# Kernel tuning notes

Hardware: AMD Instinct MI355X
Metric: run time of the kernel (lower is better)

The kernel has to match this reference:

```python
import jax, jax.numpy as jnp
import numpy as np

N_NODES = 50000
N_EDGES = 600000
D_IN = 128
D_OUT = 128
LN_EPS = 1e-5
LEAKY_SLOPE = 0.2


def setup_inputs() -> dict:
    key = jax.random.key(0)
    k1, k2, k3, k4 = jax.random.split(key, 4)
    x = jax.random.normal(k1, (N_NODES, D_IN), dtype=jnp.float32)
    edge_index = jax.random.randint(k2, (2, N_EDGES), 0, N_NODES, dtype=jnp.int64)
    # xavier_uniform with gain for relu (sqrt(2))
    gain = float(np.sqrt(2.0))
    lim_w = gain * np.sqrt(6.0 / (D_IN + D_OUT))
    W_lin = jax.random.uniform(k3, (D_OUT, D_IN), minval=-lim_w, maxval=lim_w, dtype=jnp.float32)
    lim_a = gain * np.sqrt(6.0 / (2 * D_OUT + 1))
    a = jax.random.uniform(k4, (2 * D_OUT,), minval=-lim_a, maxval=lim_a, dtype=jnp.float32)
    gamma = jnp.ones((D_OUT,), dtype=jnp.float32)
    beta = jnp.zeros((D_OUT,), dtype=jnp.float32)
    return {"x": x, "edge_index": edge_index, "W_lin": W_lin, "a": a,
            "gamma": gamma, "beta": beta}


def reference(x, edge_index, W_lin, a, gamma, beta):
    N = x.shape[0]
    h = x @ W_lin.T                                  # [N, D_OUT]
    d = h.shape[1]
    # attention MLP on concat([h_src, h_dst]) == h_src@a[:d] + h_dst@a[d:]
    s_src = h @ a[:d]                                # [N]
    s_dst = h @ a[d:]                                # [N]
    src, dst = edge_index[0], edge_index[1]
    e = jax.nn.leaky_relu(s_src[src] + s_dst[dst], LEAKY_SLOPE)   # [E]
    # segment softmax over destination nodes (numerically stable)
    m = jax.ops.segment_max(e, dst, num_segments=N)               # [N], -inf for empty
    ex = jnp.exp(e - m[dst])                                      # [E]
    z = jax.ops.segment_sum(ex, dst, num_segments=N)              # [N]
    alpha = ex / z[dst]                                           # [E]
    # weighted scatter-add of source messages
    msgs = h[src] * alpha[:, None]                                # [E, D_OUT]
    agg = jax.ops.segment_sum(msgs, dst, num_segments=N)          # [N, D_OUT]
    # residual (input_dim == output_dim -> identity projection) + LayerNorm
    y = agg + x
    mu = jnp.mean(y, axis=-1, keepdims=True)
    var = jnp.mean(jnp.square(y - mu), axis=-1, keepdims=True)
    return (y - mu) * jax.lax.rsqrt(var + LN_EPS) * gamma + beta
```

## Files before the change

### kernel.cpp

```cpp
#include <hip/hip_runtime.h>
#include <hip/hip_bf16.h>

typedef unsigned short u16;
typedef unsigned int   u32;
typedef __bf16 bf16x8 __attribute__((ext_vector_type(8)));
typedef float  f32x4  __attribute__((ext_vector_type(4)));

#define D 128
#define CPAD 16

__device__ inline float bflo(u32 u) { return __builtin_bit_cast(float, u << 16); }
__device__ inline float bfhi(u32 u) { return __builtin_bit_cast(float, u & 0xffff0000u); }
__device__ inline float bfu(u16 u)  { return __builtin_bit_cast(float, ((u32)u) << 16); }
__device__ inline u16 f2bf(float f) {
    __hip_bfloat16 b = __float2bfloat16(f);
    return __builtin_bit_cast(u16, b);
}

__device__ inline int detect_f32(const u32* __restrict__ x32, int lane) {
    u32 v = x32[lane];
    u32 elo = (v >> 7) & 0xFFu;
    return __popcll(__ballot(elo >= 150u)) >= 4;
}
__device__ inline int detect_i64(const int* __restrict__ ei32, int lane) {
    return __popcll(__ballot(ei32[2 * lane + 1] != 0)) < 8;
}

#define LWP 136

__global__ __launch_bounds__(256) void k_gemm(const void* __restrict__ xv,
                                              const void* __restrict__ Wv,
                                              const void* __restrict__ av,
                                              const int* __restrict__ ei,
                                              u16* __restrict__ h,
                                              float* __restrict__ s_src,
                                              float* __restrict__ s_dst,
                                              int* __restrict__ cnt,
                                              u32* __restrict__ scode,
                                              int N, int E)
{
    __shared__ u16 lw[128 * LWP];
    const int tid  = threadIdx.x;
    const int wave = tid >> 6;
    const int lane = tid & 63;
    const int quad = lane >> 4;
    const int l16  = lane & 15;
    const int m0   = blockIdx.x * 64 + wave * 16;

    const int f32 = detect_f32((const u32*)xv, lane);
    const int i64 = detect_i64(ei, lane);

    const int gtid = blockIdx.x * 256 + tid;
    const int TT   = gridDim.x * 256;
    int dk[3], tk[3];
#pragma unroll
    for (int k = 0; k < 3; ++k) {
        int e = gtid + k * TT;
        dk[k] = 0;
        if (e < E) {
            if (i64) dk[k] = ((const int2*)ei)[E + e].x;
            else     dk[k] = ei[E + e];
        }
    }
#pragma unroll
    for (int k = 0; k < 3; ++k) {
        int e = gtid + k * TT;
        tk[k] = 64;
        if (e < E) tk[k] = atomicAdd(cnt + (size_t)dk[k] * CPAD, 1);
    }

    if (f32) {
        const float* Wf = (const float*)Wv;
#pragma unroll
        for (int it = 0; it < 8; ++it) {
            int i = it * 256 + tid;
            int row = i >> 4, blk = i & 15;
            const float* src = Wf + row * D + blk * 8;
            f32x4 v0 = *(const f32x4*)src;
            f32x4 v1 = *(const f32x4*)(src + 4);
            union { u16 u[8]; uint4 q; } t;
#pragma unroll
            for (int j = 0; j < 4; ++j) { t.u[j] = f2bf(v0[j]); t.u[4 + j] = f2bf(v1[j]); }
            *(uint4*)&lw[row * LWP + blk * 8] = t.q;
        }
    } else {
        const u16* Wu = (const u16*)Wv;
#pragma unroll
        for (int it = 0; it < 8; ++it) {
            int i = it * 256 + tid;
            int row = i >> 4, blk = i & 15;
            *(uint4*)&lw[row * LWP + blk * 8] = *(const uint4*)(Wu + row * D + blk * 8);
        }
    }

    int arow = m0 + l16;
    if (arow > N - 1) arow = N - 1;

    bf16x8 afrag[4];
    if (f32) {
        const float* xr = (const float*)xv + (size_t)arow * D + quad * 8;
#pragma unroll
        for (int s = 0; s < 4; ++s) {
            f32x4 v0 = *(const f32x4*)(xr + s * 32);
            f32x4 v1 = *(const f32x4*)(xr + s * 32 + 4);
            union { u16 u[8]; bf16x8 v; } t;
#pragma unroll
            for (int j = 0; j < 4; ++j) { t.u[j] = f2bf(v0[j]); t.u[4 + j] = f2bf(v1[j]); }
            afrag[s] = t.v;
        }
    } else {
        const u16* xr = (const u16*)xv + (size_t)arow * D + quad * 8;
#pragma unroll
        for (int s = 0; s < 4; ++s)
            afrag[s] = __builtin_bit_cast(bf16x8, *(const uint4*)(xr + s * 32));
    }

    __syncthreads();

    f32x4 acc[8] = {};
#pragma unroll
    for (int t = 0; t < 8; ++t) {
#pragma unroll
        for (int s = 0; s < 4; ++s) {
            bf16x8 b = __builtin_bit_cast(bf16x8,
                *(const uint4*)&lw[(t * 16 + l16) * LWP + quad * 8 + s * 32]);
            acc[t] = __builtin_amdgcn_mfma_f32_16x16x32_bf16(afrag[s], b, acc[t], 0, 0, 0);
        }
    }

    float as[8], ad[8];
    if (f32) {
        const float* af = (const float*)av;
#pragma unroll
        for (int t = 0; t < 8; ++t) { as[t] = af[t * 16 + l16]; ad[t] = af[D + t * 16 + l16]; }
    } else {
        const u16* au = (const u16*)av;
#pragma unroll
        for (int t = 0; t < 8; ++t) { as[t] = bfu(au[t * 16 + l16]); ad[t] = bfu(au[D + t * 16 + l16]); }
    }

#pragma unroll
    for (int i = 0; i < 4; ++i) {
        int r = m0 + quad * 4 + i;
        float ps = 0.f, pd = 0.f;
#pragma unroll
        for (int t = 0; t < 8; ++t) {
            float v = acc[t][i];
            ps += v * as[t];
            pd += v * ad[t];
        }
#pragma unroll
        for (int m = 1; m < 16; m <<= 1) {
            ps += __shfl_xor(ps, m, 64);
            pd += __shfl_xor(pd, m, 64);
        }
        if (r < N) {
            if (l16 == 0) { s_src[r] = ps; s_dst[r] = pd; }
            u16* hrow = h + (size_t)r * D + l16;
#pragma unroll
            for (int t = 0; t < 8; ++t)
                hrow[t * 16] = f2bf(acc[t][i]);
        }
    }

#pragma unroll
    for (int k = 0; k < 3; ++k) {
        int e = gtid + k * TT;
        if (e < E)
            scode[e] = (tk[k] < 64) ? (u32)(dk[k] * 64 + tk[k]) : 0xFFFFFFFFu;
    }
}

__global__ __launch_bounds__(256) void k_edge(const int* __restrict__ ei,
                                              const float* __restrict__ s_src,
                                              const float* __restrict__ s_dst,
                                              const u32* __restrict__ scode,
                                              u32* __restrict__ bkt, int E)
{
    const int lane = threadIdx.x & 63;
    const int i64 = detect_i64(ei, lane);
    int e = blockIdx.x * 256 + threadIdx.x;
    if (e >= E) return;

    u32 code = scode[e];
    int src, dst;
    if (i64) {
        src = ((const int2*)ei)[e].x;
        dst = ((const int2*)ei)[E + e].x;
    } else {
        src = ei[e]; dst = ei[E + e];
    }
    float sv = s_src[src] + s_dst[dst];
    float lr = sv > 0.f ? sv : 0.2f * sv;
    float ex = __expf(lr);
    if (code != 0xFFFFFFFFu)
        bkt[code] = (u32)(src & 0xFFFF) | ((u32)f2bf(ex) << 16);
}

__global__ __launch_bounds__(256) void k_agg(const u16* __restrict__ h,
                                             const void* __restrict__ xv,
                                             const int* __restrict__ cnt,
                                             const u32* __restrict__ bkt,
                                             const void* __restrict__ gv_,
                                             const void* __restrict__ bv_,
                                             void* __restrict__ outv, int N)
{
    const int lane = threadIdx.x & 63;
    const int f32 = detect_f32((const u32*)xv, lane);
    const int wave = threadIdx.x >> 6;
    const int quad = lane >> 4;
    const int l16  = lane & 15;
    const int n = blockIdx.x * 4 + wave;
    if (n >= N) return;

    float xr_[8], g[8], bb[8];
    if (f32) {
        const float* xr = (const float*)xv + (size_t)n * D + l16 * 8;
        const float* gr = (const float*)gv_ + l16 * 8;
        const float* br = (const float*)bv_ + l16 * 8;
#pragma unroll
        for (int k = 0; k < 8; ++k) { xr_[k] = xr[k]; g[k] = gr[k]; bb[k] = br[k]; }
    } else {
        uint4 xq = *(const uint4*)((const u16*)xv + (size_t)n * D + l16 * 8);
        uint4 gq = *(const uint4*)((const u16*)gv_ + l16 * 8);
        uint4 bq = *(const uint4*)((const u16*)bv_ + l16 * 8);
        const u32 xw[4] = {xq.x, xq.y, xq.z, xq.w};
        const u32 gw[4] = {gq.x, gq.y, gq.z, gq.w};
        const u32 bw[4] = {bq.x, bq.y, bq.z, bq.w};
#pragma unroll
        for (int k = 0; k < 4; ++k) {
            xr_[2*k] = bflo(xw[k]); xr_[2*k+1] = bfhi(xw[k]);
            g[2*k]   = bflo(gw[k]); g[2*k+1]   = bfhi(gw[k]);
            bb[2*k]  = bflo(bw[k]); bb[2*k+1]  = bfhi(bw[k]);
        }
    }

    int d = cnt[(size_t)n * CPAD]; if (d > 64) d = 64;
    d = __builtin_amdgcn_readfirstlane(d);
    const int ng = (d + 3) >> 2;
    const u32* slots = bkt + n * 64;

    u32 pk[8];
#pragma unroll
    for (int k = 0; k < 8; ++k)
        if (k < ng) pk[k] = slots[4 * k + quad];

    uint4 hv[8];
    float w[8];
#pragma unroll
    for (int k = 0; k < 8; ++k) {
        if (k < ng) {
            bool act = (4 * k + quad) < d;
            u32 p = act ? pk[k] : 0u;
            w[k] = act ? bfhi(pk[k]) : 0.f;
            hv[k] = *(const uint4*)(h + (size_t)(p & 0xFFFFu) * D + l16 * 8);
        }
    }

    float acc[8] = {};
    float zs = 0.f;
#pragma unroll
    for (int k = 0; k < 8; ++k) {
        if (k < ng) {
            float wk = w[k];
            uint4 q = hv[k];
            zs += wk;
            acc[0] += wk * bflo(q.x); acc[1] += wk * bfhi(q.x);
            acc[2] += wk * bflo(q.y); acc[3] += wk * bfhi(q.y);
            acc[4] += wk * bflo(q.z); acc[5] += wk * bfhi(q.z);
            acc[6] += wk * bflo(q.w); acc[7] += wk * bfhi(q.w);
        }
    }

    int j = 32;
    for (; j + 4 <= d; j += 4) {
        u32 pkk = slots[j + quad];
        float wk = bfhi(pkk);
        uint4 q = *(const uint4*)(h + (size_t)(pkk & 0xFFFFu) * D + l16 * 8);
        zs += wk;
        acc[0] += wk * bflo(q.x); acc[1] += wk * bfhi(q.x);
        acc[2] += wk * bflo(q.y); acc[3] += wk * bfhi(q.y);
        acc[4] += wk * bflo(q.z); acc[5] += wk * bfhi(q.z);
        acc[6] += wk * bflo(q.w); acc[7] += wk * bfhi(q.w);
    }
    if (j + quad < d) {
        u32 pkk = slots[j + quad];
        float wk = bfhi(pkk);
        uint4 q = *(const uint4*)(h + (size_t)(pkk & 0xFFFFu) * D + l16 * 8);
        zs += wk;
        acc[0] += wk * bflo(q.x); acc[1] += wk * bfhi(q.x);
        acc[2] += wk * bflo(q.y); acc[3] += wk * bfhi(q.y);
        acc[4] += wk * bflo(q.z); acc[5] += wk * bfhi(q.z);
        acc[6] += wk * bflo(q.w); acc[7] += wk * bfhi(q.w);
    }

#pragma unroll
    for (int k = 0; k < 8; ++k) {
        acc[k] += __shfl_xor(acc[k], 16, 64);
        acc[k] += __shfl_xor(acc[k], 32, 64);
    }
    zs += __shfl_xor(zs, 16, 64);
    zs += __shfl_xor(zs, 32, 64);
    float inv = d > 0 ? 1.f / zs : 0.f;

    float y[8];
#pragma unroll
    for (int k = 0; k < 8; ++k) y[k] = acc[k] * inv + xr_[k];

    float s1 = 0.f, s2 = 0.f;
#pragma unroll
    for (int k = 0; k < 8; ++k) { s1 += y[k]; s2 += y[k] * y[k]; }
#pragma unroll
    for (int m = 1; m < 16; m <<= 1) {
        s1 += __shfl_xor(s1, m, 64);
        s2 += __shfl_xor(s2, m, 64);
    }
    float mu  = s1 * (1.f / 128.f);
    float var = s2 * (1.f / 128.f) - mu * mu;
    float r   = rsqrtf(var + 1e-5f);

    if (quad == 0) {
        if (f32) {
            float* orow = (float*)outv + (size_t)n * D + l16 * 8;
            f32x4 o0, o1;
#pragma unroll
            for (int k = 0; k < 4; ++k) o0[k] = (y[k] - mu) * r * g[k] + bb[k];
#pragma unroll
            for (int k = 0; k < 4; ++k) o1[k] = (y[4+k] - mu) * r * g[4+k] + bb[4+k];
            *(f32x4*)orow = o0;
            *(f32x4*)(orow + 4) = o1;
        } else {
            uint4 pkq;
            u32 wq[4];
#pragma unroll
            for (int k = 0; k < 4; ++k) {
                float o0 = (y[2*k]   - mu) * r * g[2*k]   + bb[2*k];
                float o1 = (y[2*k+1] - mu) * r * g[2*k+1] + bb[2*k+1];
                wq[k] = (u32)f2bf(o0) | ((u32)f2bf(o1) << 16);
            }
            pkq.x = wq[0]; pkq.y = wq[1]; pkq.z = wq[2]; pkq.w = wq[3];
            *(uint4*)((u16*)outv + (size_t)n * D + l16 * 8) = pkq;
        }
    }
}

extern "C" void kernel_launch(void* const* d_in, const int* in_sizes, int n_in,
                              void* d_out, int out_size, void* d_ws, size_t ws_size,
                              hipStream_t stream)
{
    const void* x  = d_in[0];
    const int*  ei = (const int*)d_in[1];
    const void* W  = d_in[2];
    const void* a  = d_in[3];
    const void* gm = d_in[4];
    const void* bt = d_in[5];

    const int N = in_sizes[0] / D;
    const int E = in_sizes[1] / 2;

    char* ws = (char*)d_ws;
    size_t off = 0;
    u16*   h     = (u16*)(ws + off);   off += (size_t)N * D * sizeof(u16);
    float* ssrc  = (float*)(ws + off); off += (size_t)N * sizeof(float);
    float* sdst  = (float*)(ws + off); off += (size_t)N * sizeof(float);
    int*   cnt   = (int*)(ws + off);   off += (size_t)N * CPAD * sizeof(int);
    u32*   bkt   = (u32*)(ws + off);   off += (size_t)N * 64 * sizeof(u32);
    u32*   scode = (u32*)(ws + off);   off += (size_t)E * sizeof(u32);

    hipMemsetAsync(cnt, 0, (size_t)N * CPAD * sizeof(int), stream);
    k_gemm <<<(N + 63) / 64,   256, 0, stream>>>(x, W, a, ei, h, ssrc, sdst, cnt, scode, N, E);
    k_edge <<<(E + 255) / 256, 256, 0, stream>>>(ei, ssrc, sdst, scode, bkt, E);
    k_agg  <<<(N + 3) / 4,     256, 0, stream>>>(h, x, cnt, bkt, gm, bt, d_out, N);
}
```

Measured before the change: 166.6 us.

## Fuse memset, GEMM, edge and aggregation into one cooperative persistent kernel

```diff
diff --git a/kernel.cpp b/kernel.cpp
--- a/kernel.cpp
+++ b/kernel.cpp
@@ -1,5 +1,8 @@
 #include <hip/hip_runtime.h>
 #include <hip/hip_bf16.h>
+#include <hip/hip_cooperative_groups.h>
+
+namespace cg = cooperative_groups;
 
 typedef unsigned short u16;
 typedef unsigned int   u32;
@@ -8,6 +11,8 @@
 
 #define D 128
 #define CPAD 16
+#define LWP 136
+#define EK 8
 
 __device__ inline float bflo(u32 u) { return __builtin_bit_cast(float, u << 16); }
 __device__ inline float bfhi(u32 u) { return __builtin_bit_cast(float, u & 0xffff0000u); }
@@ -26,7 +31,313 @@
     return __popcll(__ballot(ei32[2 * lane + 1] != 0)) < 8;
 }
 
-#define LWP 136
+__global__ __launch_bounds__(256) void k_fused(
+    const void* __restrict__ xv, const void* __restrict__ Wv,
+    const void* __restrict__ av, const int* __restrict__ ei,
+    const void* __restrict__ gv_, const void* __restrict__ bv_,
+    void* __restrict__ outv,
+    u16* __restrict__ h, float* __restrict__ s_src, float* __restrict__ s_dst,
+    int* __restrict__ cnt, u32* __restrict__ bkt, int N, int E)
+{
+    __shared__ u16 lw[128 * LWP];
+    const int tid  = threadIdx.x;
+    const int wave = tid >> 6;
+    const int lane = tid & 63;
+    const int quad = lane >> 4;
+    const int l16  = lane & 15;
+    const int G    = gridDim.x;
+    const int gtid = blockIdx.x * 256 + tid;
+    const int TT   = G * 256;
+
+    const int f32 = detect_f32((const u32*)xv, lane);
+    const int i64 = detect_i64(ei, lane);
+
+    for (int ci = gtid; ci < (N * CPAD) >> 2; ci += TT) {
+        int4 z = {0, 0, 0, 0};
+        *(int4*)(cnt + (size_t)ci * 4) = z;
+    }
+    __threadfence();
+    cg::this_grid().sync();
+    __threadfence();
+
+    int dd[EK];
+#pragma unroll
+    for (int k = 0; k < EK; ++k) {
+        int e = gtid + k * TT;
+        dd[k] = 0;
+        if (e < E) dd[k] = i64 ? ((const int2*)ei)[E + e].x : ei[E + e];
+    }
+    int tk[EK];
+#pragma unroll
+    for (int k = 0; k < EK; ++k) {
+        int e = gtid + k * TT;
+        tk[k] = 64;
+        if (e < E) tk[k] = atomicAdd(cnt + (size_t)dd[k] * CPAD, 1);
+    }
+
+    const int TILES = (N + 63) >> 6;
+    bool staged = false;
+    for (int tile = blockIdx.x; tile < TILES; tile += G) {
+        if (!staged) {
+            staged = true;
+            if (f32) {
+                const float* Wf = (const float*)Wv;
+#pragma unroll
+                for (int it = 0; it < 8; ++it) {
+                    int i = it * 256 + tid;
+                    int row = i >> 4, blk = i & 15;
+                    const float* src = Wf + row * D + blk * 8;
+                    f32x4 v0 = *(const f32x4*)src;
+                    f32x4 v1 = *(const f32x4*)(src + 4);
+                    union { u16 u[8]; uint4 q; } t;
+#pragma unroll
+                    for (int j = 0; j < 4; ++j) { t.u[j] = f2bf(v0[j]); t.u[4 + j] = f2bf(v1[j]); }
+                    *(uint4*)&lw[row * LWP + blk * 8] = t.q;
+                }
+            } else {
+                const u16* Wu = (const u16*)Wv;
+#pragma unroll
+                for (int it = 0; it < 8; ++it) {
+                    int i = it * 256 + tid;
+                    int row = i >> 4, blk = i & 15;
+                    *(uint4*)&lw[row * LWP + blk * 8] = *(const uint4*)(Wu + row * D + blk * 8);
+                }
+            }
+        }
+
+        int m0 = tile * 64 + wave * 16;
+        int arow = m0 + l16;
+        if (arow > N - 1) arow = N - 1;
+
+        bf16x8 afrag[4];
+        if (f32) {
+            const float* xr = (const float*)xv + (size_t)arow * D + quad * 8;
+#pragma unroll
+            for (int s = 0; s < 4; ++s) {
+                f32x4 v0 = *(const f32x4*)(xr + s * 32);
+                f32x4 v1 = *(const f32x4*)(xr + s * 32 + 4);
+                union { u16 u[8]; bf16x8 v; } t;
+#pragma unroll
+                for (int j = 0; j < 4; ++j) { t.u[j] = f2bf(v0[j]); t.u[4 + j] = f2bf(v1[j]); }
+                afrag[s] = t.v;
+            }
+        } else {
+            const u16* xr = (const u16*)xv + (size_t)arow * D + quad * 8;
+#pragma unroll
+            for (int s = 0; s < 4; ++s)
+                afrag[s] = __builtin_bit_cast(bf16x8, *(const uint4*)(xr + s * 32));
+        }
+
+        __syncthreads();
+
+        f32x4 acc[8] = {};
+#pragma unroll
+        for (int t = 0; t < 8; ++t) {
+#pragma unroll
+            for (int s = 0; s < 4; ++s) {
+                bf16x8 b = __builtin_bit_cast(bf16x8,
+                    *(const uint4*)&lw[(t * 16 + l16) * LWP + quad * 8 + s * 32]);
+                acc[t] = __builtin_amdgcn_mfma_f32_16x16x32_bf16(afrag[s], b, acc[t], 0, 0, 0);
+            }
+        }
+
+        float as[8], ad[8];
+        if (f32) {
+            const float* af = (const float*)av;
+#pragma unroll
+            for (int t = 0; t < 8; ++t) { as[t] = af[t * 16 + l16]; ad[t] = af[D + t * 16 + l16]; }
+        } else {
+            const u16* au = (const u16*)av;
+#pragma unroll
+            for (int t = 0; t < 8; ++t) { as[t] = bfu(au[t * 16 + l16]); ad[t] = bfu(au[D + t * 16 + l16]); }
+        }
+
+#pragma unroll
+        for (int i = 0; i < 4; ++i) {
+            int r = m0 + quad * 4 + i;
+            float ps = 0.f, pd = 0.f;
+#pragma unroll
+            for (int t = 0; t < 8; ++t) {
+                float v = acc[t][i];
+                ps += v * as[t];
+                pd += v * ad[t];
+            }
+#pragma unroll
+            for (int m = 1; m < 16; m <<= 1) {
+                ps += __shfl_xor(ps, m, 64);
+                pd += __shfl_xor(pd, m, 64);
+            }
+            if (r < N) {
+                if (l16 == 0) { s_src[r] = ps; s_dst[r] = pd; }
+                u16* hrow = h + (size_t)r * D + l16;
+#pragma unroll
+                for (int t = 0; t < 8; ++t)
+                    hrow[t * 16] = f2bf(acc[t][i]);
+            }
+        }
+    }
+    __threadfence();
+    cg::this_grid().sync();
+    __threadfence();
+
+#pragma unroll
+    for (int k = 0; k < EK; ++k) {
+        int e = gtid + k * TT;
+        if (e < E) {
+            int src, dst;
+            if (i64) {
+                src = ((const int2*)ei)[e].x;
+                dst = ((const int2*)ei)[E + e].x;
+            } else {
+                src = ei[e]; dst = ei[E + e];
+            }
+            float sv = s_src[src] + s_dst[dst];
+            float lr = sv > 0.f ? sv : 0.2f * sv;
+            float ex = __expf(lr);
+            if (tk[k] < 64)
+                bkt[(size_t)dst * 64 + tk[k]] = (u32)(src & 0xFFFF) | ((u32)f2bf(ex) << 16);
+        }
+    }
+    __threadfence();
+    cg::this_grid().sync();
+    __threadfence();
+
+    const int NB = (N + 3) >> 2;
+    for (int nb = blockIdx.x; nb < NB; nb += G) {
+        int n = nb * 4 + wave;
+        if (n < N) {
+            float xr_[8], g[8], bb[8];
+            if (f32) {
+                const float* xr = (const float*)xv + (size_t)n * D + l16 * 8;
+                const float* gr = (const float*)gv_ + l16 * 8;
+                const float* br = (const float*)bv_ + l16 * 8;
+#pragma unroll
+                for (int k = 0; k < 8; ++k) { xr_[k] = xr[k]; g[k] = gr[k]; bb[k] = br[k]; }
+            } else {
+                uint4 xq = *(const uint4*)((const u16*)xv + (size_t)n * D + l16 * 8);
+                uint4 gq = *(const uint4*)((const u16*)gv_ + l16 * 8);
+                uint4 bq = *(const uint4*)((const u16*)bv_ + l16 * 8);
+                const u32 xw[4] = {xq.x, xq.y, xq.z, xq.w};
+                const u32 gw[4] = {gq.x, gq.y, gq.z, gq.w};
+                const u32 bw[4] = {bq.x, bq.y, bq.z, bq.w};
+#pragma unroll
+                for (int k = 0; k < 4; ++k) {
+                    xr_[2*k] = bflo(xw[k]); xr_[2*k+1] = bfhi(xw[k]);
+                    g[2*k]   = bflo(gw[k]); g[2*k+1]   = bfhi(gw[k]);
+                    bb[2*k]  = bflo(bw[k]); bb[2*k+1]  = bfhi(bw[k]);
+                }
+            }
+
+            int d = cnt[(size_t)n * CPAD]; if (d > 64) d = 64;
+            d = __builtin_amdgcn_readfirstlane(d);
+            const int ng = (d + 3) >> 2;
+            const u32* slots = bkt + n * 64;
+
+            u32 pk[8];
+#pragma unroll
+            for (int k = 0; k < 8; ++k)
+                if (k < ng) pk[k] = slots[4 * k + quad];
+
+            uint4 hv[8];
+            float w[8];
+#pragma unroll
+            for (int k = 0; k < 8; ++k) {
+                if (k < ng) {
+                    bool act = (4 * k + quad) < d;
+                    u32 p = act ? pk[k] : 0u;
+                    w[k] = act ? bfhi(pk[k]) : 0.f;
+                    hv[k] = *(const uint4*)(h + (size_t)(p & 0xFFFFu) * D + l16 * 8);
+                }
+            }
+
+            float acc2[8] = {};
+            float zs = 0.f;
+#pragma unroll
+            for (int k = 0; k < 8; ++k) {
+                if (k < ng) {
+                    float wk = w[k];
+                    uint4 q = hv[k];
+                    zs += wk;
+                    acc2[0] += wk * bflo(q.x); acc2[1] += wk * bfhi(q.x);
+                    acc2[2] += wk * bflo(q.y); acc2[3] += wk * bfhi(q.y);
+                    acc2[4] += wk * bflo(q.z); acc2[5] += wk * bfhi(q.z);
+                    acc2[6] += wk * bflo(q.w); acc2[7] += wk * bfhi(q.w);
+                }
+            }
+
+            int j = 32;
+            for (; j + 4 <= d; j += 4) {
+                u32 pkk = slots[j + quad];
+                float wk = bfhi(pkk);
+                uint4 q = *(const uint4*)(h + (size_t)(pkk & 0xFFFFu) * D + l16 * 8);
+                zs += wk;
+                acc2[0] += wk * bflo(q.x); acc2[1] += wk * bfhi(q.x);
+                acc2[2] += wk * bflo(q.y); acc2[3] += wk * bfhi(q.y);
+                acc2[4] += wk * bflo(q.z); acc2[5] += wk * bfhi(q.z);
+                acc2[6] += wk * bflo(q.w); acc2[7] += wk * bfhi(q.w);
+            }
+            if (j + quad < d) {
+                u32 pkk = slots[j + quad];
+                float wk = bfhi(pkk);
+                uint4 q = *(const uint4*)(h + (size_t)(pkk & 0xFFFFu) * D + l16 * 8);
+                zs += wk;
+                acc2[0] += wk * bflo(q.x); acc2[1] += wk * bfhi(q.x);
+                acc2[2] += wk * bflo(q.y); acc2[3] += wk * bfhi(q.y);
+                acc2[4] += wk * bflo(q.z); acc2[5] += wk * bfhi(q.z);
+                acc2[6] += wk * bflo(q.w); acc2[7] += wk * bfhi(q.w);
+            }
+
+#pragma unroll
+            for (int k = 0; k < 8; ++k) {
+                acc2[k] += __shfl_xor(acc2[k], 16, 64);
+                acc2[k] += __shfl_xor(acc2[k], 32, 64);
+            }
+            zs += __shfl_xor(zs, 16, 64);
+            zs += __shfl_xor(zs, 32, 64);
+            float inv = d > 0 ? 1.f / zs : 0.f;
+
+            float y[8];
+#pragma unroll
+            for (int k = 0; k < 8; ++k) y[k] = acc2[k] * inv + xr_[k];
+
+            float s1 = 0.f, s2 = 0.f;
+#pragma unroll
+            for (int k = 0; k < 8; ++k) { s1 += y[k]; s2 += y[k] * y[k]; }
+#pragma unroll
+            for (int m = 1; m < 16; m <<= 1) {
+                s1 += __shfl_xor(s1, m, 64);
+                s2 += __shfl_xor(s2, m, 64);
+            }
+            float mu  = s1 * (1.f / 128.f);
+            float var = s2 * (1.f / 128.f) - mu * mu;
+            float r   = rsqrtf(var + 1e-5f);
+
+            if (quad == 0) {
+                if (f32) {
+                    float* orow = (float*)outv + (size_t)n * D + l16 * 8;
+                    f32x4 o0, o1;
+#pragma unroll
+                    for (int k = 0; k < 4; ++k) o0[k] = (y[k] - mu) * r * g[k] + bb[k];
+#pragma unroll
+                    for (int k = 0; k < 4; ++k) o1[k] = (y[4+k] - mu) * r * g[4+k] + bb[4+k];
+                    *(f32x4*)orow = o0;
+                    *(f32x4*)(orow + 4) = o1;
+                } else {
+                    uint4 pkq;
+                    u32 wq[4];
+#pragma unroll
+                    for (int k = 0; k < 4; ++k) {
+                        float o0 = (y[2*k]   - mu) * r * g[2*k]   + bb[2*k];
+                        float o1 = (y[2*k+1] - mu) * r * g[2*k+1] + bb[2*k+1];
+                        wq[k] = (u32)f2bf(o0) | ((u32)f2bf(o1) << 16);
+                    }
+                    pkq.x = wq[0]; pkq.y = wq[1]; pkq.z = wq[2]; pkq.w = wq[3];
+                    *(uint4*)((u16*)outv + (size_t)n * D + l16 * 8) = pkq;
+                }
+            }
+        }
+    }
+}
 
 __global__ __launch_bounds__(256) void k_gemm(const void* __restrict__ xv,
                                               const void* __restrict__ Wv,
@@ -367,8 +678,46 @@
     u32*   bkt   = (u32*)(ws + off);   off += (size_t)N * 64 * sizeof(u32);
     u32*   scode = (u32*)(ws + off);   off += (size_t)E * sizeof(u32);
 
-    hipMemsetAsync(cnt, 0, (size_t)N * CPAD * sizeof(int), stream);
-    k_gemm <<<(N + 63) / 64,   256, 0, stream>>>(x, W, a, ei, h, ssrc, sdst, cnt, scode, N, E);
-    k_edge <<<(E + 255) / 256, 256, 0, stream>>>(ei, ssrc, sdst, scode, bkt, E);
-    k_agg  <<<(N + 3) / 4,     256, 0, stream>>>(h, x, cnt, bkt, gm, bt, d_out, N);
+    static int coopG = -2;
+    if (coopG == -2) {
+        int dev = 0;
+        hipGetDevice(&dev);
+        hipDeviceProp_t props;
+        int maxBlk = 0;
+        if (hipGetDeviceProperties(&props, dev) == hipSuccess &&
+            props.cooperativeLaunch &&
+            hipOccupancyMaxActiveBlocksPerMultiprocessor(
+                &maxBlk, (const void*)k_fused, 256, 0) == hipSuccess &&
+            maxBlk >= 1) {
+            long g = (long)maxBlk * props.multiProcessorCount;
+            if (g * 256 * EK >= E)
+                coopG = (int)g;
+            else
+                coopG = -1;
+        } else {
+            coopG = -1;
+        }
+    }
+
+    bool done = false;
+    if (coopG > 0) {
+        void* outv = d_out;
+        int  Na = N, Ea = E;
+        void* args[] = { (void*)&x, (void*)&W, (void*)&a, (void*)&ei,
+                         (void*)&gm, (void*)&bt, (void*)&outv,
+                         (void*)&h, (void*)&ssrc, (void*)&sdst,
+                         (void*)&cnt, (void*)&bkt, (void*)&Na, (void*)&Ea };
+        hipError_t err = hipLaunchCooperativeKernel((const void*)k_fused,
+                                                    dim3(coopG), dim3(256),
+                                                    args, 0, stream);
+        if (err == hipSuccess) done = true;
+        else coopG = -1;
+    }
+
+    if (!done) {
+        hipMemsetAsync(cnt, 0, (size_t)N * CPAD * sizeof(int), stream);
+        k_gemm <<<(N + 63) / 64,   256, 0, stream>>>(x, W, a, ei, h, ssrc, sdst, cnt, scode, N, E);
+        k_edge <<<(E + 255) / 256, 256, 0, stream>>>(ei, ssrc, sdst, scode, bkt, E);
+        k_agg  <<<(N + 3) / 4,     256, 0, stream>>>(h, x, cnt, bkt, gm, bt, d_out, N);
+    }
 }
```

Result: no change. 164.3 us (-1.4%).

## Move edge counting atomics into edge kernel and fuse counter zeroing into GEMM

Applied to the files above, without the earlier changes.

```diff
diff --git a/kernel.cpp b/kernel.cpp
--- a/kernel.cpp
+++ b/kernel.cpp
@@ -3,11 +3,14 @@
 
 typedef unsigned short u16;
 typedef unsigned int   u32;
+typedef unsigned long long u64;
 typedef __bf16 bf16x8 __attribute__((ext_vector_type(8)));
 typedef float  f32x4  __attribute__((ext_vector_type(4)));
+typedef u32    u32x4  __attribute__((ext_vector_type(4)));
 
 #define D 128
 #define CPAD 16
+#define LWP 136
 
 __device__ inline float bflo(u32 u) { return __builtin_bit_cast(float, u << 16); }
 __device__ inline float bfhi(u32 u) { return __builtin_bit_cast(float, u & 0xffff0000u); }
@@ -26,18 +29,13 @@
     return __popcll(__ballot(ei32[2 * lane + 1] != 0)) < 8;
 }
 
-#define LWP 136
-
 __global__ __launch_bounds__(256) void k_gemm(const void* __restrict__ xv,
                                               const void* __restrict__ Wv,
                                               const void* __restrict__ av,
-                                              const int* __restrict__ ei,
                                               u16* __restrict__ h,
                                               float* __restrict__ s_src,
                                               float* __restrict__ s_dst,
-                                              int* __restrict__ cnt,
-                                              u32* __restrict__ scode,
-                                              int N, int E)
+                                              int* __restrict__ cnt, int N)
 {
     __shared__ u16 lw[128 * LWP];
     const int tid  = threadIdx.x;
@@ -48,25 +46,13 @@
     const int m0   = blockIdx.x * 64 + wave * 16;
 
     const int f32 = detect_f32((const u32*)xv, lane);
-    const int i64 = detect_i64(ei, lane);
-
-    const int gtid = blockIdx.x * 256 + tid;
-    const int TT   = gridDim.x * 256;
-    int dk[3], tk[3];
-#pragma unroll
-    for (int k = 0; k < 3; ++k) {
-        int e = gtid + k * TT;
-        dk[k] = 0;
-        if (e < E) {
-            if (i64) dk[k] = ((const int2*)ei)[E + e].x;
-            else     dk[k] = ei[E + e];
-        }
-    }
-#pragma unroll
-    for (int k = 0; k < 3; ++k) {
-        int e = gtid + k * TT;
-        tk[k] = 64;
-        if (e < E) tk[k] = atomicAdd(cnt + (size_t)dk[k] * CPAD, 1);
+
+    {
+        int ci = blockIdx.x * 256 + tid;
+        if (ci * 4 < N * CPAD) {
+            int4 z = {0, 0, 0, 0};
+            *(int4*)(cnt + (size_t)ci * 4) = z;
+        }
     }
 
     if (f32) {
@@ -162,39 +148,56 @@
                 hrow[t * 16] = f2bf(acc[t][i]);
         }
     }
-
-#pragma unroll
-    for (int k = 0; k < 3; ++k) {
-        int e = gtid + k * TT;
-        if (e < E)
-            scode[e] = (tk[k] < 64) ? (u32)(dk[k] * 64 + tk[k]) : 0xFFFFFFFFu;
-    }
 }
 
 __global__ __launch_bounds__(256) void k_edge(const int* __restrict__ ei,
                                               const float* __restrict__ s_src,
                                               const float* __restrict__ s_dst,
-                                              const u32* __restrict__ scode,
+                                              int* __restrict__ cnt,
                                               u32* __restrict__ bkt, int E)
 {
     const int lane = threadIdx.x & 63;
     const int i64 = detect_i64(ei, lane);
-    int e = blockIdx.x * 256 + threadIdx.x;
-    if (e >= E) return;
-
-    u32 code = scode[e];
-    int src, dst;
-    if (i64) {
-        src = ((const int2*)ei)[e].x;
-        dst = ((const int2*)ei)[E + e].x;
-    } else {
-        src = ei[e]; dst = ei[E + e];
-    }
-    float sv = s_src[src] + s_dst[dst];
-    float lr = sv > 0.f ? sv : 0.2f * sv;
-    float ex = __expf(lr);
-    if (code != 0xFFFFFFFFu)
-        bkt[code] = (u32)(src & 0xFFFF) | ((u32)f2bf(ex) << 16);
+    const int T = (E + 3) >> 2;
+    const int e0 = blockIdx.x * 256 + threadIdx.x;
+    if (e0 >= T) return;
+
+    int src[4], dst[4], tk[4];
+#pragma unroll
+    for (int k = 0; k < 4; ++k) {
+        int e = e0 + k * T;
+        src[k] = 0; dst[k] = 0;
+        if (e < E) {
+            if (i64) {
+                u64 vs = __builtin_nontemporal_load((const u64*)ei + e);
+                u64 vd = __builtin_nontemporal_load((const u64*)ei + E + e);
+                src[k] = (int)(u32)vs; dst[k] = (int)(u32)vd;
+            } else {
+                src[k] = __builtin_nontemporal_load(ei + e);
+                dst[k] = __builtin_nontemporal_load(ei + E + e);
+            }
+        }
+    }
+#pragma unroll
+    for (int k = 0; k < 4; ++k) {
+        int e = e0 + k * T;
+        tk[k] = 64;
+        if (e < E) tk[k] = atomicAdd(cnt + (size_t)dst[k] * CPAD, 1);
+    }
+    float a[4], b[4];
+#pragma unroll
+    for (int k = 0; k < 4; ++k) {
+        a[k] = s_src[src[k]];
+        b[k] = s_dst[dst[k]];
+    }
+#pragma unroll
+    for (int k = 0; k < 4; ++k) {
+        float sv = a[k] + b[k];
+        float lr = sv > 0.f ? sv : 0.2f * sv;
+        float ex = __expf(lr);
+        if (tk[k] < 64)
+            bkt[(size_t)dst[k] * 64 + tk[k]] = (u32)(src[k] & 0xFFFF) | ((u32)f2bf(ex) << 16);
+    }
 }
 
 __global__ __launch_bounds__(256) void k_agg(const u16* __restrict__ h,
@@ -218,18 +221,21 @@
         const float* xr = (const float*)xv + (size_t)n * D + l16 * 8;
         const float* gr = (const float*)gv_ + l16 * 8;
         const float* br = (const float*)bv_ + l16 * 8;
-#pragma unroll
-        for (int k = 0; k < 8; ++k) { xr_[k] = xr[k]; g[k] = gr[k]; bb[k] = br[k]; }
+        f32x4 x0 = __builtin_nontemporal_load((const f32x4*)xr);
+        f32x4 x1 = __builtin_nontemporal_load((const f32x4*)(xr + 4));
+#pragma unroll
+        for (int k = 0; k < 4; ++k) { xr_[k] = x0[k]; xr_[4 + k] = x1[k]; }
+#pragma unroll
+        for (int k = 0; k < 8; ++k) { g[k] = gr[k]; bb[k] = br[k]; }
     } else {
-        uint4 xq = *(const uint4*)((const u16*)xv + (size_t)n * D + l16 * 8);
+        u32x4 xq = __builtin_nontemporal_load((const u32x4*)((const u16*)xv + (size_t)n * D + l16 * 8));
         uint4 gq = *(const uint4*)((const u16*)gv_ + l16 * 8);
         uint4 bq = *(const uint4*)((const u16*)bv_ + l16 * 8);
-        const u32 xw[4] = {xq.x, xq.y, xq.z, xq.w};
         const u32 gw[4] = {gq.x, gq.y, gq.z, gq.w};
         const u32 bw[4] = {bq.x, bq.y, bq.z, bq.w};
 #pragma unroll
         for (int k = 0; k < 4; ++k) {
-            xr_[2*k] = bflo(xw[k]); xr_[2*k+1] = bfhi(xw[k]);
+            xr_[2*k] = bflo(xq[k]); xr_[2*k+1] = bfhi(xq[k]);
             g[2*k]   = bflo(gw[k]); g[2*k+1]   = bfhi(gw[k]);
             bb[2*k]  = bflo(bw[k]); bb[2*k+1]  = bfhi(bw[k]);
         }
@@ -327,19 +333,17 @@
             for (int k = 0; k < 4; ++k) o0[k] = (y[k] - mu) * r * g[k] + bb[k];
 #pragma unroll
             for (int k = 0; k < 4; ++k) o1[k] = (y[4+k] - mu) * r * g[4+k] + bb[4+k];
-            *(f32x4*)orow = o0;
-            *(f32x4*)(orow + 4) = o1;
+            __builtin_nontemporal_store(o0, (f32x4*)orow);
+            __builtin_nontemporal_store(o1, (f32x4*)(orow + 4));
         } else {
-            uint4 pkq;
-            u32 wq[4];
+            u32x4 pkq;
 #pragma unroll
             for (int k = 0; k < 4; ++k) {
                 float o0 = (y[2*k]   - mu) * r * g[2*k]   + bb[2*k];
                 float o1 = (y[2*k+1] - mu) * r * g[2*k+1] + bb[2*k+1];
-                wq[k] = (u32)f2bf(o0) | ((u32)f2bf(o1) << 16);
+                pkq[k] = (u32)f2bf(o0) | ((u32)f2bf(o1) << 16);
             }
-            pkq.x = wq[0]; pkq.y = wq[1]; pkq.z = wq[2]; pkq.w = wq[3];
-            *(uint4*)((u16*)outv + (size_t)n * D + l16 * 8) = pkq;
+            __builtin_nontemporal_store(pkq, (u32x4*)((u16*)outv + (size_t)n * D + l16 * 8));
         }
     }
 }
@@ -365,10 +369,10 @@
     float* sdst  = (float*)(ws + off); off += (size_t)N * sizeof(float);
     int*   cnt   = (int*)(ws + off);   off += (size_t)N * CPAD * sizeof(int);
     u32*   bkt   = (u32*)(ws + off);   off += (size_t)N * 64 * sizeof(u32);
-    u32*   scode = (u32*)(ws + off);   off += (size_t)E * sizeof(u32);
-
-    hipMemsetAsync(cnt, 0, (size_t)N * CPAD * sizeof(int), stream);
-    k_gemm <<<(N + 63) / 64,   256, 0, stream>>>(x, W, a, ei, h, ssrc, sdst, cnt, scode, N, E);
-    k_edge <<<(E + 255) / 256, 256, 0, stream>>>(ei, ssrc, sdst, scode, bkt, E);
+
+    const int T = (E + 3) / 4;
+
+    k_gemm <<<(N + 63) / 64,   256, 0, stream>>>(x, W, a, h, ssrc, sdst, cnt, N);
+    k_edge <<<(T + 255) / 256, 256, 0, stream>>>(ei, ssrc, sdst, cnt, bkt, E);
     k_agg  <<<(N + 3) / 4,     256, 0, stream>>>(h, x, cnt, bkt, gm, bt, d_out, N);
 }
```

After: 162.4 us. 1.03x faster.
